# Performance work log

Measured on AMD Instinct MI355X. Metric: run time of the kernel, lower is better.

## Reference

```python
import jax, jax.numpy as jnp
import numpy as np

D_MODEL = 1024
N_HEADS = 16
HEAD_DIM = D_MODEL // N_HEADS
ROPE_BASE = 10000.0


def _rope_cos_sin(t, dtype):
    # inv_freq over half the head dim, standard RoPE (GPT-NeoX style)
    inv_freq = 1.0 / (ROPE_BASE ** (jnp.arange(0, HEAD_DIM, 2, dtype=jnp.float32) / HEAD_DIM))
    freqs = jnp.arange(t, dtype=jnp.float32)[:, None] * inv_freq[None, :]  # [t, hd/2]
    emb = jnp.concatenate([freqs, freqs], axis=-1)  # [t, hd]
    return jnp.cos(emb).astype(dtype), jnp.sin(emb).astype(dtype)


def _rotate_half(x):
    x1, x2 = jnp.split(x, 2, axis=-1)
    return jnp.concatenate([-x2, x1], axis=-1)


def _apply_rope(x, cos, sin):
    # x: [b, h, t, hd]; cos/sin: [t, hd]
    return x * cos[None, None] + _rotate_half(x) * sin[None, None]


def setup_inputs() -> dict:
    key = jax.random.key(0)
    kx, kqkv, kout = jax.random.split(key, 3)
    x = jax.random.normal(kx, (4, 2048, D_MODEL), dtype=jnp.float32)
    scale = 1.0 / np.sqrt(D_MODEL)
    Wqkv = jax.random.normal(kqkv, (D_MODEL, 3 * D_MODEL), dtype=jnp.float32) * scale
    Wout = jax.random.normal(kout, (D_MODEL, D_MODEL), dtype=jnp.float32) * scale
    return {"x": x, "Wqkv": Wqkv, "Wout": Wout}


def reference(x, Wqkv, Wout):
    b, t, _ = x.shape
    qkv = (x @ Wqkv).reshape(b, t, 3, N_HEADS, HEAD_DIM)
    q, k, v = qkv[:, :, 0], qkv[:, :, 1], qkv[:, :, 2]  # [b, t, h, hd]
    q = q.transpose(0, 2, 1, 3)  # [b, h, t, hd]
    k = k.transpose(0, 2, 1, 3)
    v = v.transpose(0, 2, 1, 3)
    cos, sin = _rope_cos_sin(t, x.dtype)
    q = _apply_rope(q, cos, sin)
    k = _apply_rope(k, cos, sin)
    # causal SDPA
    scores = jnp.einsum("bhqd,bhkd->bhqk", q, k) / np.sqrt(HEAD_DIM)
    causal = jnp.tril(jnp.ones((t, t), dtype=bool))
    scores = jnp.where(causal[None, None], scores, jnp.finfo(scores.dtype).min)
    attn = jax.nn.softmax(scores, axis=-1)
    out = jnp.einsum("bhqk,bhkd->bhqd", attn, v)
    out = out.transpose(0, 2, 1, 3).reshape(b, t, D_MODEL)
    return out @ Wout
```

## Files before the change

### kernel.cpp

```cpp
#include <hip/hip_runtime.h>
#include <cstdint>
#include <cstddef>

typedef __bf16 bf16;
typedef __bf16 bf16x8 __attribute__((ext_vector_type(8)));
typedef __bf16 bf16x4 __attribute__((ext_vector_type(4)));
typedef float  f32x4  __attribute__((ext_vector_type(4)));
typedef float  f32x16 __attribute__((ext_vector_type(16)));

#define MFMA16(a, b, c) __builtin_amdgcn_mfma_f32_16x16x32_bf16((a), (b), (c), 0, 0, 0)
#define MFMA32(a, b, c) __builtin_amdgcn_mfma_f32_32x32x16_bf16((a), (b), (c), 0, 0, 0)

static constexpr int BB   = 4;
static constexpr int TT   = 2048;
static constexpr int DM   = 1024;
static constexpr int NH   = 16;
static constexpr int HD   = 64;
static constexpr int TOK  = BB * TT;
static constexpr int NQKV = 3 * DM;

__device__ inline void gload16(const void* g, void* l) {
    __builtin_amdgcn_global_load_lds((const __attribute__((address_space(1))) void*)g,
                                     (__attribute__((address_space(3))) void*)l, 16, 0, 0);
}

__device__ inline int swz(int x) { return x ^ ((x >> 3) & 0x70); }

__global__ void k_cvt(const float* __restrict__ in, bf16* __restrict__ out, int n) {
    int i = (blockIdx.x * blockDim.x + threadIdx.x) * 4;
    if (i >= n) return;
    float4 v = *(const float4*)(in + i);
    bf16x4 o;
    o[0] = (bf16)v.x; o[1] = (bf16)v.y; o[2] = (bf16)v.z; o[3] = (bf16)v.w;
    *(bf16x4*)(out + i) = o;
}

__global__ void k_transpose_cvt(const float* __restrict__ in, bf16* __restrict__ out,
                                int R, int C) {
    __shared__ bf16 tl[64 * 72];
    int tid = threadIdx.x;
    int c0 = blockIdx.x * 64, r0 = blockIdx.y * 64;
#pragma unroll
    for (int rep = 0; rep < 4; rep++) {
        int r = rep * 16 + (tid >> 4);
        int c = (tid & 15) * 4;
        float4 v = *(const float4*)(in + (size_t)(r0 + r) * C + c0 + c);
        tl[r * 72 + c + 0] = (bf16)v.x;
        tl[r * 72 + c + 1] = (bf16)v.y;
        tl[r * 72 + c + 2] = (bf16)v.z;
        tl[r * 72 + c + 3] = (bf16)v.w;
    }
    __syncthreads();
#pragma unroll
    for (int rep = 0; rep < 4; rep++) {
        int cc = rep * 16 + (tid >> 4);
        int rr = (tid & 15) * 4;
        bf16x4 o;
        o[0] = tl[(rr + 0) * 72 + cc];
        o[1] = tl[(rr + 1) * 72 + cc];
        o[2] = tl[(rr + 2) * 72 + cc];
        o[3] = tl[(rr + 3) * 72 + cc];
        *(bf16x4*)(out + (size_t)(c0 + cc) * R + r0 + rr) = o;
    }
}

__global__ void k_rope_tab(float* __restrict__ ct, float* __restrict__ st) {
    int i = blockIdx.x * blockDim.x + threadIdx.x;
    int t = i >> 5, j = i & 31;
    float invf = powf(10000.0f, -(float)j * (1.0f / 32.0f));
    float a = (float)t * invf;
    ct[i] = cosf(a);
    st[i] = sinf(a);
}

template <int MODE>
__global__ __launch_bounds__(256) void k_gemm_bt(
    const bf16* __restrict__ A, const bf16* __restrict__ Bt,
    int M, int N, int K,
    float* __restrict__ outF,
    bf16* __restrict__ qbuf, bf16* __restrict__ kbuf, bf16* __restrict__ vbuf,
    const float* __restrict__ ct, const float* __restrict__ st, float qscale) {
    __shared__ bf16 lA[2][128 * 64];
    __shared__ bf16 lB[2][128 * 64];
    int tid = threadIdx.x;
    int l = tid & 63, wid = tid >> 6;
    int wm = wid >> 1, wn = wid & 1;
    int bn = blockIdx.x, bm = blockIdx.y;
    const char* AbB = (const char*)(A + (size_t)bm * 128 * K);
    const char* BbB = (const char*)(Bt + (size_t)bn * 128 * K);
    const size_t KB = (size_t)K * 2;
    f32x4 acc[4][4] = {};

#define GSTAGE(nb, kt) do {                                                                \
    _Pragma("unroll") for (int i = 0; i < 4; i++) {                                        \
        int cb = (wid * 4 + i) * 1024;               \
        int Xs = swz(cb + l * 16);                   \
        gload16(AbB + (size_t)(Xs >> 7) * KB + (size_t)(kt) * 2 + (Xs & 127),              \
                (char*)lA[nb] + cb);                                                       \
        gload16(BbB + (size_t)(Xs >> 7) * KB + (size_t)(kt) * 2 + (Xs & 127),              \
                (char*)lB[nb] + cb);                                                       \
    }                                                                                      \
} while (0)

    GSTAGE(0, 0);
    __syncthreads();
    int cur = 0;
    int nsteps = K >> 6;
    for (int t = 0; t < nsteps; t++) {
        if (t + 1 < nsteps) GSTAGE(cur ^ 1, (t + 1) << 6);
#pragma unroll
        for (int kk = 0; kk < 2; kk++) {
            bf16x8 af[4], bfr[4];
#pragma unroll
            for (int mi = 0; mi < 4; mi++) {
                int rr = wm * 64 + mi * 16 + (l & 15);
                int L = rr * 128 + (kk * 32 + (l >> 4) * 8) * 2;
                af[mi] = *(const bf16x8*)((const char*)lA[cur] + swz(L));
            }
#pragma unroll
            for (int ni = 0; ni < 4; ni++) {
                int rr = wn * 64 + ni * 16 + (l & 15);
                int L = rr * 128 + (kk * 32 + (l >> 4) * 8) * 2;
                bfr[ni] = *(const bf16x8*)((const char*)lB[cur] + swz(L));
            }
#pragma unroll
            for (int mi = 0; mi < 4; mi++)
#pragma unroll
                for (int ni = 0; ni < 4; ni++)
                    acc[mi][ni] = MFMA16(af[mi], bfr[ni], acc[mi][ni]);
        }
        __syncthreads();
        cur ^= 1;
    }
#undef GSTAGE

    if (MODE == 2) {
#pragma unroll
        for (int mi = 0; mi < 4; mi++) {
            int m0 = bm * 128 + wm * 64 + mi * 16 + ((l >> 4) << 2);
#pragma unroll
            for (int ni = 0; ni < 4; ni++) {
                int n = bn * 128 + wn * 64 + ni * 16 + (l & 15);
#pragma unroll
                for (int rj = 0; rj < 4; rj++)
                    outF[(size_t)(m0 + rj) * N + n] = acc[mi][ni][rj];
            }
        }
    } else {
        int n0 = bn * 128 + wn * 64;
        int sQ = n0 >> 10;
        int h = (n0 & 1023) >> 6;
        if (sQ == 2) {
#pragma unroll
            for (int ni = 0; ni < 4; ni++) {
                int d = ni * 16 + (l & 15);
#pragma unroll
                for (int mi = 0; mi < 4; mi++) {
                    int m0 = bm * 128 + wm * 64 + mi * 16 + ((l >> 4) << 2);
                    int b = m0 >> 11, t0 = m0 & 2047;
                    bf16x4 pv;
#pragma unroll
                    for (int rj = 0; rj < 4; rj++) pv[rj] = (bf16)acc[mi][ni][rj];
                    *(bf16x4*)(vbuf + ((size_t)((b * NH + h) * HD + d)) * TT + t0) = pv;
                }
            }
        } else {
            float qs = (sQ == 0) ? qscale : 1.0f;
            bf16* obuf = (sQ == 0) ? qbuf : kbuf;
#pragma unroll
            for (int mi = 0; mi < 4; mi++) {
                int m0 = bm * 128 + wm * 64 + mi * 16 + ((l >> 4) << 2);
                int b = m0 >> 11, t0 = m0 & 2047;
#pragma unroll
                for (int rj = 0; rj < 4; rj++) {
                    int t = t0 + rj;
                    bf16* dst = obuf + ((size_t)(b * NH + h) * TT + t) * HD;
                    const float* crow = ct + t * 32;
                    const float* srow = st + t * 32;
#pragma unroll
                    for (int ni2 = 0; ni2 < 2; ni2++) {
                        int d = ni2 * 16 + (l & 15);
                        float cs = crow[d], sn = srow[d];
                        float a  = acc[mi][ni2][rj];
                        float b2 = acc[mi][ni2 + 2][rj];
                        dst[d]      = (bf16)(qs * (a  * cs - b2 * sn));
                        dst[d + 32] = (bf16)(qs * (b2 * cs + a  * sn));
                    }
                }
            }
        }
    }
}

__global__ __launch_bounds__(256, 2) void k_attn(
    const bf16* __restrict__ Q, const bf16* __restrict__ K,
    const bf16* __restrict__ Vt, bf16* __restrict__ O) {
    __shared__ bf16 lK[2][4096];
    __shared__ bf16 lV[2][4096];
    __shared__ bf16 lP[8192];
    int tid = threadIdx.x;
    int l = tid & 63, w = tid >> 6;
    int bx = blockIdx.x, by = blockIdx.y;
    int bh = bx * 8 + (by >> 3);
    int p = by & 7;
    const char* KbB = (const char*)(K + (size_t)bh * TT * HD);
    const char* VbB = (const char*)(Vt + (size_t)bh * HD * TT);
    int b = bh >> 4, h = bh & 15;

    bf16x8 ones;
#pragma unroll
    for (int e = 0; e < 8; e++) ones[e] = (bf16)1.0f;

#define STAGE_KV(nb, j) do {                                                               \
    int X0_ = w * 1024 + l * 16;                                                           \
    const char* Kj_ = KbB + (size_t)(j) * 8192;                                            \
    gload16(Kj_ + swz(X0_),        (char*)lK[nb] + w * 1024);                              \
    gload16(Kj_ + swz(X0_ + 4096), (char*)lK[nb] + w * 1024 + 4096);                       \
    int o0_ = swz(X0_), o1_ = swz(X0_ + 4096);                                             \
    gload16(VbB + (size_t)(o0_ >> 7) * (TT * 2) + (size_t)(j) * 128 + (o0_ & 127),         \
            (char*)lV[nb] + w * 1024);                                                     \
    gload16(VbB + (size_t)(o1_ >> 7) * (TT * 2) + (size_t)(j) * 128 + (o1_ & 127),         \
            (char*)lV[nb] + w * 1024 + 4096);                                              \
} while (0)

    for (int half = 0; half < 2; half++) {
        int s = (half == 0) ? (15 - p) : p;
        int r0 = s * 128;
        int nblk = 2 * s + 2;
        int wrow = r0 + w * 32;
        const bf16* Qb = Q + ((size_t)bh * TT + wrow) * HD;
        bf16x8 qa[4];
#pragma unroll
        for (int kc = 0; kc < 4; kc++)
            qa[kc] = *(const bf16x8*)(Qb + (size_t)(l & 31) * HD + kc * 16 + (l >> 5) * 8);

        f32x16 oacc[2] = {};
        f32x16 lacc = {};

        STAGE_KV(0, 0);
        __syncthreads();
        int cur = 0;
        for (int j = 0; j < nblk; j++) {
            if (j + 1 < nblk) STAGE_KV(cur ^ 1, j + 1);
            if (j * 64 <= wrow + 31) {
                f32x16 sc[2];
#pragma unroll
                for (int r = 0; r < 16; r++) { sc[0][r] = -16.0f; sc[1][r] = -16.0f; }
                __builtin_amdgcn_s_setprio(1);
#pragma unroll
                for (int kc = 0; kc < 4; kc++)
#pragma unroll
                    for (int nj = 0; nj < 2; nj++) {
                        int rr = nj * 32 + (l & 31);
                        int L = rr * 128 + ((kc * 16 + (l >> 5) * 8) * 2 ^ ((rr & 7) << 4));
                        bf16x8 kb = *(const bf16x8*)((const char*)lK[cur] + L);
                        sc[nj] = MFMA32(qa[kc], kb, sc[nj]);
                    }
                __builtin_amdgcn_s_setprio(0);
                if (j * 64 + 63 > wrow) {
#pragma unroll
                    for (int nj = 0; nj < 2; nj++) {
                        int colg = j * 64 + nj * 32 + (l & 31);
#pragma unroll
                        for (int r = 0; r < 16; r++) {
                            int rowq = wrow + (r & 3) + 8 * (r >> 2) + 4 * (l >> 5);
                            if (colg > rowq) sc[nj][r] = -1e30f;
                        }
                    }
                }
                {
                    int prB = w * 32 + 4 * (l >> 5);
#pragma unroll
                    for (int nj = 0; nj < 2; nj++) {
                        int pcB = (nj * 32 + (l & 31)) * 2;
#pragma unroll
                        for (int r = 0; r < 16; r++) {
                            int row = prB + (r & 3) + 8 * (r >> 2);
                            *(bf16*)((char*)lP + row * 128 + (pcB ^ ((row & 7) << 4)))
                                = (bf16)exp2f(sc[nj][r]);
                        }
                    }
                }
                __builtin_amdgcn_s_setprio(1);
#pragma unroll
                for (int kc = 0; kc < 4; kc++) {
                    int pr = w * 32 + (l & 31);
                    bf16x8 pa = *(const bf16x8*)((const char*)lP + pr * 128
                                 + ((kc * 32 + (l >> 5) * 16) ^ ((pr & 7) << 4)));
                    lacc = MFMA32(pa, ones, lacc);
#pragma unroll
                    for (int dt = 0; dt < 2; dt++) {
                        int dd = dt * 32 + (l & 31);
                        int L = dd * 128 + ((kc * 16 + (l >> 5) * 8) * 2 ^ ((dd & 7) << 4));
                        bf16x8 vbf = *(const bf16x8*)((const char*)lV[cur] + L);
                        oacc[dt] = MFMA32(pa, vbf, oacc[dt]);
                    }
                }
                __builtin_amdgcn_s_setprio(0);
            }
            __syncthreads();
            cur ^= 1;
        }
#pragma unroll
        for (int r = 0; r < 16; r++) {
            int rq = (r & 3) + 8 * (r >> 2) + 4 * (l >> 5);
            int t = wrow + rq;
            float inv = 1.0f / lacc[r];
            size_t base = ((size_t)b * TT + t) * DM + h * HD;
#pragma unroll
            for (int dt = 0; dt < 2; dt++)
                O[base + dt * 32 + (l & 31)] = (bf16)(oacc[dt][r] * inv);
        }
    }
#undef STAGE_KV
}

extern "C" void kernel_launch(void* const* d_in, const int* in_sizes, int n_in,
                              void* d_out, int out_size, void* d_ws, size_t ws_size,
                              hipStream_t stream) {
    const float* x    = (const float*)d_in[0];
    const float* Wqkv = (const float*)d_in[1];
    const float* Wout = (const float*)d_in[2];
    float* out = (float*)d_out;

    char* ws = (char*)d_ws;
    size_t off = 0;
    auto alloc = [&](size_t bytes) {
        void* p = ws + off;
        off += (bytes + 255) & ~(size_t)255;
        return p;
    };
    bf16* xb    = (bf16*)alloc((size_t)TOK * DM * 2);
    bf16* wqkvt = (bf16*)alloc((size_t)NQKV * DM * 2);
    bf16* woutt = (bf16*)alloc((size_t)DM * DM * 2);
    bf16* qr    = (bf16*)alloc((size_t)TOK * DM * 2);
    bf16* kr    = (bf16*)alloc((size_t)TOK * DM * 2);
    bf16* vt    = (bf16*)alloc((size_t)TOK * DM * 2);
    bf16* ob    = (bf16*)alloc((size_t)TOK * DM * 2);
    float* ct   = (float*)alloc((size_t)TT * 32 * 4);
    float* st   = (float*)alloc((size_t)TT * 32 * 4);
    (void)ws_size; (void)in_sizes; (void)n_in; (void)out_size;

    k_cvt<<<TOK * DM / 4 / 256, 256, 0, stream>>>(x, xb, TOK * DM);
    k_transpose_cvt<<<dim3(NQKV / 64, DM / 64), 256, 0, stream>>>(Wqkv, wqkvt, DM, NQKV);
    k_transpose_cvt<<<dim3(DM / 64, DM / 64), 256, 0, stream>>>(Wout, woutt, DM, DM);
    k_rope_tab<<<TT * 32 / 256, 256, 0, stream>>>(ct, st);
    k_gemm_bt<1><<<dim3(NQKV / 128, TOK / 128), 256, 0, stream>>>(
        xb, wqkvt, TOK, NQKV, DM, nullptr, qr, kr, vt,
        ct, st, 0.125f * 1.4426950408889634f);
    k_attn<<<dim3(8, BB * NH), 256, 0, stream>>>(qr, kr, vt, ob);
    k_gemm_bt<2><<<dim3(DM / 128, TOK / 128), 256, 0, stream>>>(
        ob, woutt, TOK, DM, DM, out, nullptr, nullptr, nullptr,
        nullptr, nullptr, 0.0f);
}
```

Baseline: 189.0 us.

## Keep softmax probabilities in registers via transposed QK^T and permlane swap

The attention kernel now computes S^T (K as the A operand) so each lane holds a query column. After exp2 it packs the probabilities to bf16 and uses v_permlane32_swap to form the PV MFMA A-operand directly, which removes the LDS round trip through the lP buffer. With the smaller LDS footprint, launch bounds rise to 3 blocks per CU. The grid is also reshaped to one 128-row query tile per block (1024 blocks, heaviest first) instead of pairing two tiles per block, trading the explicit load balancing for more parallelism.

Result: slower. 201.2 us (+6.5%).

```diff
diff --git a/kernel.cpp b/kernel.cpp
--- a/kernel.cpp
+++ b/kernel.cpp
@@ -5,8 +5,10 @@
 typedef __bf16 bf16;
 typedef __bf16 bf16x8 __attribute__((ext_vector_type(8)));
 typedef __bf16 bf16x4 __attribute__((ext_vector_type(4)));
+typedef __bf16 bf16x2 __attribute__((ext_vector_type(2)));
 typedef float  f32x4  __attribute__((ext_vector_type(4)));
 typedef float  f32x16 __attribute__((ext_vector_type(16)));
+typedef int    i32x4  __attribute__((ext_vector_type(4)));
 
 #define MFMA16(a, b, c) __builtin_amdgcn_mfma_f32_16x16x32_bf16((a), (b), (c), 0, 0, 0)
 #define MFMA32(a, b, c) __builtin_amdgcn_mfma_f32_32x32x16_bf16((a), (b), (c), 0, 0, 0)
@@ -25,6 +27,11 @@
 }
 
 __device__ inline int swz(int x) { return x ^ ((x >> 3) & 0x70); }
+
+__device__ inline int pk2(float a, float b) {
+    bf16x2 t; t[0] = (bf16)a; t[1] = (bf16)b;
+    return __builtin_bit_cast(int, t);
+}
 
 __global__ void k_cvt(const float* __restrict__ in, bf16* __restrict__ out, int n) {
     int i = (blockIdx.x * blockDim.x + threadIdx.x) * 4;
@@ -192,17 +199,16 @@
     }
 }
 
-__global__ __launch_bounds__(256, 2) void k_attn(
+__global__ __launch_bounds__(256, 3) void k_attn(
     const bf16* __restrict__ Q, const bf16* __restrict__ K,
     const bf16* __restrict__ Vt, bf16* __restrict__ O) {
     __shared__ bf16 lK[2][4096];
     __shared__ bf16 lV[2][4096];
-    __shared__ bf16 lP[8192];
     int tid = threadIdx.x;
     int l = tid & 63, w = tid >> 6;
     int bx = blockIdx.x, by = blockIdx.y;
-    int bh = bx * 8 + (by >> 3);
-    int p = by & 7;
+    int bh = bx * 8 + (by >> 4);
+    int s = 15 - (by & 15);
     const char* KbB = (const char*)(K + (size_t)bh * TT * HD);
     const char* VbB = (const char*)(Vt + (size_t)bh * HD * TT);
     int b = bh >> 4, h = bh & 15;
@@ -223,94 +229,88 @@
             (char*)lV[nb] + w * 1024 + 4096);                                              \
 } while (0)
 
-    for (int half = 0; half < 2; half++) {
-        int s = (half == 0) ? (15 - p) : p;
-        int r0 = s * 128;
-        int nblk = 2 * s + 2;
-        int wrow = r0 + w * 32;
-        const bf16* Qb = Q + ((size_t)bh * TT + wrow) * HD;
-        bf16x8 qa[4];
-#pragma unroll
-        for (int kc = 0; kc < 4; kc++)
-            qa[kc] = *(const bf16x8*)(Qb + (size_t)(l & 31) * HD + kc * 16 + (l >> 5) * 8);
-
-        f32x16 oacc[2] = {};
-        f32x16 lacc = {};
-
-        STAGE_KV(0, 0);
+    int r0 = s * 128;
+    int nblk = 2 * s + 2;
+    int wrow = r0 + w * 32;
+    const bf16* Qb = Q + ((size_t)bh * TT + wrow) * HD;
+    bf16x8 qa[4];
+#pragma unroll
+    for (int kc = 0; kc < 4; kc++)
+        qa[kc] = *(const bf16x8*)(Qb + (size_t)(l & 31) * HD + kc * 16 + (l >> 5) * 8);
+
+    f32x16 oacc[2] = {};
+    f32x16 lacc = {};
+
+    STAGE_KV(0, 0);
+    __syncthreads();
+    int cur = 0;
+    for (int j = 0; j < nblk; j++) {
+        if (j + 1 < nblk) STAGE_KV(cur ^ 1, j + 1);
+        if (j * 64 <= wrow + 31) {
+            f32x16 sc[2];
+#pragma unroll
+            for (int r = 0; r < 16; r++) { sc[0][r] = -16.0f; sc[1][r] = -16.0f; }
+            __builtin_amdgcn_s_setprio(1);
+#pragma unroll
+            for (int kc = 0; kc < 4; kc++)
+#pragma unroll
+                for (int nj = 0; nj < 2; nj++) {
+                    int rr = nj * 32 + (l & 31);
+                    int L = rr * 128 + ((kc * 16 + (l >> 5) * 8) * 2 ^ ((rr & 7) << 4));
+                    bf16x8 kb = *(const bf16x8*)((const char*)lK[cur] + L);
+                    sc[nj] = MFMA32(kb, qa[kc], sc[nj]);
+                }
+            __builtin_amdgcn_s_setprio(0);
+            if (j * 64 + 63 > wrow) {
+                int q = wrow + (l & 31);
+#pragma unroll
+                for (int nj = 0; nj < 2; nj++)
+#pragma unroll
+                    for (int r = 0; r < 16; r++) {
+                        int kvg = j * 64 + nj * 32 + (r & 3) + 8 * (r >> 2) + 4 * (l >> 5);
+                        if (kvg > q) sc[nj][r] = -1e30f;
+                    }
+            }
+#pragma unroll
+            for (int nj = 0; nj < 2; nj++)
+#pragma unroll
+                for (int r = 0; r < 16; r++)
+                    sc[nj][r] = exp2f(sc[nj][r]);
+            __builtin_amdgcn_s_setprio(1);
+#pragma unroll
+            for (int c = 0; c < 4; c++) {
+                const int nj = c >> 1, rb = (c & 1) * 8;
+                int w0 = pk2(sc[nj][rb + 0], sc[nj][rb + 1]);
+                int w1 = pk2(sc[nj][rb + 2], sc[nj][rb + 3]);
+                int w2 = pk2(sc[nj][rb + 4], sc[nj][rb + 5]);
+                int w3 = pk2(sc[nj][rb + 6], sc[nj][rb + 7]);
+                asm("v_permlane32_swap_b32 %0, %1" : "+v"(w0), "+v"(w2));
+                asm("v_permlane32_swap_b32 %0, %1" : "+v"(w1), "+v"(w3));
+                i32x4 fw; fw[0] = w0; fw[1] = w1; fw[2] = w2; fw[3] = w3;
+                bf16x8 pa = __builtin_bit_cast(bf16x8, fw);
+                lacc = MFMA32(pa, ones, lacc);
+#pragma unroll
+                for (int dt = 0; dt < 2; dt++) {
+                    int dd = dt * 32 + (l & 31);
+                    int L = dd * 128 + ((c * 16 + (l >> 5) * 8) * 2 ^ ((dd & 7) << 4));
+                    bf16x8 vbf = *(const bf16x8*)((const char*)lV[cur] + L);
+                    oacc[dt] = MFMA32(pa, vbf, oacc[dt]);
+                }
+            }
+            __builtin_amdgcn_s_setprio(0);
+        }
         __syncthreads();
-        int cur = 0;
-        for (int j = 0; j < nblk; j++) {
-            if (j + 1 < nblk) STAGE_KV(cur ^ 1, j + 1);
-            if (j * 64 <= wrow + 31) {
-                f32x16 sc[2];
-#pragma unroll
-                for (int r = 0; r < 16; r++) { sc[0][r] = -16.0f; sc[1][r] = -16.0f; }
-                __builtin_amdgcn_s_setprio(1);
-#pragma unroll
-                for (int kc = 0; kc < 4; kc++)
-#pragma unroll
-                    for (int nj = 0; nj < 2; nj++) {
-                        int rr = nj * 32 + (l & 31);
-                        int L = rr * 128 + ((kc * 16 + (l >> 5) * 8) * 2 ^ ((rr & 7) << 4));
-                        bf16x8 kb = *(const bf16x8*)((const char*)lK[cur] + L);
-                        sc[nj] = MFMA32(qa[kc], kb, sc[nj]);
-                    }
-                __builtin_amdgcn_s_setprio(0);
-                if (j * 64 + 63 > wrow) {
-#pragma unroll
-                    for (int nj = 0; nj < 2; nj++) {
-                        int colg = j * 64 + nj * 32 + (l & 31);
-#pragma unroll
-                        for (int r = 0; r < 16; r++) {
-                            int rowq = wrow + (r & 3) + 8 * (r >> 2) + 4 * (l >> 5);
-                            if (colg > rowq) sc[nj][r] = -1e30f;
-                        }
-                    }
-                }
-                {
-                    int prB = w * 32 + 4 * (l >> 5);
-#pragma unroll
-                    for (int nj = 0; nj < 2; nj++) {
-                        int pcB = (nj * 32 + (l & 31)) * 2;
-#pragma unroll
-                        for (int r = 0; r < 16; r++) {
-                            int row = prB + (r & 3) + 8 * (r >> 2);
-                            *(bf16*)((char*)lP + row * 128 + (pcB ^ ((row & 7) << 4)))
-                                = (bf16)exp2f(sc[nj][r]);
-                        }
-                    }
-                }
-                __builtin_amdgcn_s_setprio(1);
-#pragma unroll
-                for (int kc = 0; kc < 4; kc++) {
-                    int pr = w * 32 + (l & 31);
-                    bf16x8 pa = *(const bf16x8*)((const char*)lP + pr * 128
-                                 + ((kc * 32 + (l >> 5) * 16) ^ ((pr & 7) << 4)));
-                    lacc = MFMA32(pa, ones, lacc);
-#pragma unroll
-                    for (int dt = 0; dt < 2; dt++) {
-                        int dd = dt * 32 + (l & 31);
-                        int L = dd * 128 + ((kc * 16 + (l >> 5) * 8) * 2 ^ ((dd & 7) << 4));
-                        bf16x8 vbf = *(const bf16x8*)((const char*)lV[cur] + L);
-                        oacc[dt] = MFMA32(pa, vbf, oacc[dt]);
-                    }
-                }
-                __builtin_amdgcn_s_setprio(0);
-            }
-            __syncthreads();
-            cur ^= 1;
-        }
-#pragma unroll
-        for (int r = 0; r < 16; r++) {
-            int rq = (r & 3) + 8 * (r >> 2) + 4 * (l >> 5);
-            int t = wrow + rq;
-            float inv = 1.0f / lacc[r];
-            size_t base = ((size_t)b * TT + t) * DM + h * HD;
-#pragma unroll
-            for (int dt = 0; dt < 2; dt++)
-                O[base + dt * 32 + (l & 31)] = (bf16)(oacc[dt][r] * inv);
-        }
+        cur ^= 1;
+    }
+#pragma unroll
+    for (int r = 0; r < 16; r++) {
+        int rq = (r & 3) + 8 * (r >> 2) + 4 * (l >> 5);
+        int t = wrow + rq;
+        float inv = 1.0f / lacc[r];
+        size_t base = ((size_t)b * TT + t) * DM + h * HD;
+#pragma unroll
+        for (int dt = 0; dt < 2; dt++)
+            O[base + dt * 32 + (l & 31)] = (bf16)(oacc[dt][r] * inv);
     }
 #undef STAGE_KV
 }
@@ -348,7 +348,7 @@
     k_gemm_bt<1><<<dim3(NQKV / 128, TOK / 128), 256, 0, stream>>>(
         xb, wqkvt, TOK, NQKV, DM, nullptr, qr, kr, vt,
         ct, st, 0.125f * 1.4426950408889634f);
-    k_attn<<<dim3(8, BB * NH), 256, 0, stream>>>(qr, kr, vt, ob);
+    k_attn<<<dim3(8, 128), 256, 0, stream>>>(qr, kr, vt, ob);
     k_gemm_bt<2><<<dim3(DM / 128, TOK / 128), 256, 0, stream>>>(
         ob, woutt, TOK, DM, DM, out, nullptr, nullptr, nullptr,
         nullptr, nullptr, 0.0f);
```
